# Performance work log

Measured on AMD Instinct MI355X. Metric: run time of the kernel, lower is better.

## Reference

```python
import jax, jax.numpy as jnp
import numpy as np

N_SVC = 100000
N_EP = 100000
E = 300000
D = 128
H = 128


def _sage(x_src, x_dst, edge_index, Wl, bl, Wr, n_dst):
    """PyG SAGEConv default: mean neighbor aggr, lin_l(aggr) + lin_r(x_dst)."""
    src, dst = edge_index[0], edge_index[1]
    msg = x_src[src]                                        # [E, D] gather
    sums = jax.ops.segment_sum(msg, dst, num_segments=n_dst)  # [n_dst, D]
    cnt = jax.ops.segment_sum(jnp.ones((msg.shape[0], 1), msg.dtype), dst,
                              num_segments=n_dst)             # [n_dst, 1]
    mean = sums / jnp.maximum(cnt, 1.0)
    return mean @ Wl.T + bl + x_dst @ Wr.T                  # [n_dst, H]


def setup_inputs() -> dict:
    key = jax.random.key(0)
    ks = jax.random.split(key, 16)
    scale = 1.0 / np.sqrt(D)
    inp = {
        "x_service": jax.random.normal(ks[0], (N_SVC, D), jnp.float32),
        "x_endpoint": jax.random.normal(ks[1], (N_EP, D), jnp.float32),
        "ei_calls": jax.random.randint(ks[2], (2, E), 0, N_SVC),   # svc -> svc
        "ei_has": jax.random.randint(ks[3], (2, E), 0, N_SVC),     # svc -> ep (dst < N_EP too)
        "ei_belongs": jax.random.randint(ks[4], (2, E), 0, N_EP),  # ep -> svc
        "Wl_calls": jax.random.normal(ks[5], (H, D), jnp.float32) * scale,
        "bl_calls": jnp.zeros((H,), jnp.float32),
        "Wr_calls": jax.random.normal(ks[6], (H, D), jnp.float32) * scale,
        "Wl_has": jax.random.normal(ks[7], (H, D), jnp.float32) * scale,
        "bl_has": jnp.zeros((H,), jnp.float32),
        "Wr_has": jax.random.normal(ks[8], (H, D), jnp.float32) * scale,
        "Wl_belongs": jax.random.normal(ks[9], (H, D), jnp.float32) * scale,
        "bl_belongs": jnp.zeros((H,), jnp.float32),
        "Wr_belongs": jax.random.normal(ks[10], (H, D), jnp.float32) * scale,
    }
    return inp


def reference(x_service, x_endpoint, ei_calls, ei_has, ei_belongs,
              Wl_calls, bl_calls, Wr_calls,
              Wl_has, bl_has, Wr_has,
              Wl_belongs, bl_belongs, Wr_belongs):
    # edge type (service, calls, service) -> service output
    out_calls = _sage(x_service, x_service, ei_calls, Wl_calls, bl_calls, Wr_calls, N_SVC)
    # edge type (endpoint, belongs, service) -> service output
    out_belongs = _sage(x_endpoint, x_service, ei_belongs, Wl_belongs, bl_belongs, Wr_belongs, N_SVC)
    # edge type (service, has, endpoint) -> endpoint output
    out_has = _sage(x_service, x_endpoint, ei_has, Wl_has, bl_has, Wr_has, N_EP)
    # HeteroConv aggr='sum': sum per destination node type
    out_service = out_calls + out_belongs
    out_endpoint = out_has
    return out_service, out_endpoint
```

## Files before the change

### kernel.cpp

```cpp
#include <hip/hip_runtime.h>

#define DF 128
#define CAP 24

typedef __bf16 bf16x8 __attribute__((ext_vector_type(8)));
typedef float f32x4 __attribute__((ext_vector_type(4)));
typedef unsigned short ushort8v __attribute__((ext_vector_type(8)));

__device__ __forceinline__ unsigned short f2bf(float f) {
    union { float f; unsigned int u; } v; v.f = f;
    unsigned int r = v.u + 0x7FFFu + ((v.u >> 16) & 1u);
    return (unsigned short)(r >> 16);
}
__device__ __forceinline__ float bf2f(unsigned short u) {
    union { unsigned int u; float f; } v; v.u = ((unsigned int)u) << 16;
    return v.f;
}

__global__ __launch_bounds__(256)
void prep_kernel(
                 const int* __restrict__ ei_calls, int E1,
                 const int* __restrict__ ei_belongs, int E2,
                 const int* __restrict__ ei_has, int E3,
                 int* __restrict__ cnt, int* __restrict__ slots,
                 const float* __restrict__ x_service,
                 const float* __restrict__ x_endpoint,
                 unsigned short* __restrict__ xb_svc,
                 unsigned short* __restrict__ xb_ep,
                 int n_svc, int n_ep,
                 const float* __restrict__ Wl_calls, const float* __restrict__ Wr_calls,
                 const float* __restrict__ Wl_belongs, const float* __restrict__ Wr_belongs,
                 const float* __restrict__ Wl_has, const float* __restrict__ Wr_has,
                 const float* __restrict__ bl_calls, const float* __restrict__ bl_belongs,
                 const float* __restrict__ bl_has,
                 unsigned short* __restrict__ Bp_svc, unsigned short* __restrict__ Bp_ep,
                 float* __restrict__ bias_svc, float* __restrict__ bias_ep,
                 int B_fill, int B_pack)
{
    int b = blockIdx.x;

    if (b < B_fill) {
        int e = b * 256 + threadIdx.x;
        int Etot = E1 + E2 + E3;
        if (e >= Etot) return;
        int s, d, base;
        if (e < E1)           { s = ei_calls[e]; d = ei_calls[E1 + e]; base = 0; }
        else if (e < E1 + E2) { int el = e - E1; s = ei_belongs[el]; d = ei_belongs[E2 + el]; base = n_svc; }
        else                  { int el = e - E1 - E2; s = ei_has[el]; d = ei_has[E3 + el]; base = 2 * n_svc; }
        int g = base + d;
        int pos = atomicAdd(cnt + g, 1);
        if (pos < CAP) slots[(size_t)g * CAP + pos] = s;
        return;
    }
    b -= B_fill;

    if (b < B_pack) {
        int t = b * 256 + threadIdx.x;
        const int SV = 12 * 8 * 64 * 8;
        const int EPN = 8 * 8 * 64 * 8;
        if (t < SV) {
            int j = t & 7, lane = (t >> 3) & 63, ct = (t >> 9) & 7, kt = t >> 12;
            int k = kt * 32 + (lane >> 4) * 8 + j;
            int n = ct * 16 + (lane & 15);
            float v;
            if (k < 128)       v = Wl_calls[n * DF + k];
            else if (k < 256)  v = Wl_belongs[n * DF + (k - 128)];
            else               v = Wr_calls[n * DF + (k - 256)] + Wr_belongs[n * DF + (k - 256)];
            Bp_svc[t] = f2bf(v);
        } else if (t < SV + EPN) {
            int t2 = t - SV;
            int j = t2 & 7, lane = (t2 >> 3) & 63, ct = (t2 >> 9) & 7, kt = t2 >> 12;
            int k = kt * 32 + (lane >> 4) * 8 + j;
            int n = ct * 16 + (lane & 15);
            float v = (k < 128) ? Wl_has[n * DF + k] : Wr_has[n * DF + (k - 128)];
            Bp_ep[t2] = f2bf(v);
        }
        if (t < 128) bias_svc[t] = bl_calls[t] + bl_belongs[t];
        else if (t < 256) bias_ep[t - 128] = bl_has[t - 128];
        return;
    }
    b -= B_pack;

    int tid = b * 256 + threadIdx.x;
    int node = tid >> 5;
    int c4 = (tid & 31) << 2;
    if (node < n_svc) {
        float4 v = *reinterpret_cast<const float4*>(x_service + (size_t)node * DF + c4);
        ushort4 o; o.x = f2bf(v.x); o.y = f2bf(v.y); o.z = f2bf(v.z); o.w = f2bf(v.w);
        *reinterpret_cast<ushort4*>(xb_svc + (size_t)node * DF + c4) = o;
    } else if (node < n_svc + n_ep) {
        int ne = node - n_svc;
        float4 v = *reinterpret_cast<const float4*>(x_endpoint + (size_t)ne * DF + c4);
        ushort4 o; o.x = f2bf(v.x); o.y = f2bf(v.y); o.z = f2bf(v.z); o.w = f2bf(v.w);
        *reinterpret_cast<ushort4*>(xb_ep + (size_t)ne * DF + c4) = o;
    }
}

template <int MODE>
__global__ __launch_bounds__(512, 4)
void fused_gemm(const unsigned short* __restrict__ xb_svc,
                const unsigned short* __restrict__ xb_ep,
                const int* __restrict__ cnt,
                const int* __restrict__ slots,
                const unsigned short* __restrict__ Bpack,
                const float* __restrict__ bias,
                float* __restrict__ out,
                int n_svc, int n_ep)
{
    constexpr int MK      = (MODE == 0) ? 256 : 128;
    constexpr int KSTEPS  = (MODE == 0) ? 12 : 8;
    constexpr int MKSTEPS = MK / 32;
    constexpr int ROWS    = 64;
    constexpr int NG      = (MODE == 0) ? 2 * ROWS : ROWS;
    constexpr int NI      = NG * 16 / 512;

    __shared__ unsigned short smean[ROWS * MK];

    const int M = (MODE == 0) ? n_svc : n_ep;
    const int row_base = blockIdx.x * ROWS;

    const int lane16 = threadIdx.x & 15;
    const int c8 = lane16 << 3;

    int degA[NI];
    int gA[NI];
    const unsigned short* srcA[NI];
    unsigned short* dstA[NI];

#pragma unroll
    for (int it = 0; it < NI; ++it) {
        int gl   = (it * 512 + threadIdx.x) >> 4;
        int node = gl & (ROWS - 1);
        int t    = gl / ROWS;
        int chunk = lane16 + t * 16;
        dstA[it] = smean + node * MK + ((chunk ^ (node & 7)) << 3);
        int gnode = row_base + node;
        int gn_c  = gnode < M ? gnode : M - 1;
        int g;
        if (MODE == 0) {
            g = (t == 0) ? gn_c : (n_svc + gn_c);
            srcA[it] = (t == 0) ? xb_svc : xb_ep;
        } else {
            g = 2 * n_svc + gn_c;
            srcA[it] = xb_svc;
        }
        gA[it] = g;
        int d = cnt[g];
        if (gnode >= M) d = 0;
        if (d > CAP) d = CAP;
        degA[it] = d;
    }

    int4 s4[NI];
#pragma unroll
    for (int it = 0; it < NI; ++it)
        s4[it] = *reinterpret_cast<const int4*>(slots + (size_t)gA[it] * CAP);

    int idxA[NI][4];
#pragma unroll
    for (int it = 0; it < NI; ++it) {
        int d = degA[it];
        idxA[it][0] = (0 < d) ? s4[it].x : 0;
        idxA[it][1] = (1 < d) ? s4[it].y : 0;
        idxA[it][2] = (2 < d) ? s4[it].z : 0;
        idxA[it][3] = (3 < d) ? s4[it].w : 0;
    }

    ushort8v vb0[4], vb1[4];
#pragma unroll
    for (int j = 0; j < 4; ++j)
        vb0[j] = *reinterpret_cast<const ushort8v*>(
            srcA[0] + (size_t)idxA[0][j] * DF + c8);

#pragma unroll
    for (int it = 0; it < NI; ++it) {
        if (it + 1 < NI) {
#pragma unroll
            for (int j = 0; j < 4; ++j) {
                const ushort8v* p = reinterpret_cast<const ushort8v*>(
                    srcA[it + 1] + (size_t)idxA[it + 1][j] * DF + c8);
                if ((it & 1) == 0) vb1[j] = *p; else vb0[j] = *p;
            }
        }
        float acc[8];
#pragma unroll
        for (int q = 0; q < 8; ++q) acc[q] = 0.f;
#pragma unroll
        for (int j = 0; j < 4; ++j) {
            if (j < degA[it]) {
                ushort8v v = ((it & 1) == 0) ? vb0[j] : vb1[j];
#pragma unroll
                for (int q = 0; q < 8; ++q) acc[q] += bf2f(v[q]);
            }
        }
        if (degA[it] <= 4) {
            float inv = 1.0f / (float)max(degA[it], 1);
            ushort8v o;
#pragma unroll
            for (int q = 0; q < 8; ++q) o[q] = f2bf(acc[q] * inv);
            *reinterpret_cast<ushort8v*>(dstA[it]) = o;
        }
    }

#pragma unroll
    for (int it = 0; it < NI; ++it) {
        int deg = degA[it];
        if (deg > 4) {
            const int* sp = slots + (size_t)gA[it] * CAP;
            const unsigned short* src = srcA[it];
            float acc[8];
#pragma unroll
            for (int q = 0; q < 8; ++q) acc[q] = 0.f;
            for (int i0 = 0; i0 < deg; i0 += 8) {
                int idx[8];
#pragma unroll
                for (int j = 0; j < 8; ++j) {
                    int ii = i0 + j;
                    if (ii > deg - 1) ii = deg - 1;
                    idx[j] = sp[ii];
                }
                ushort8v v[8];
#pragma unroll
                for (int j = 0; j < 8; ++j)
                    v[j] = *reinterpret_cast<const ushort8v*>(
                        src + (size_t)idx[j] * DF + c8);
                int nv = deg - i0;
#pragma unroll
                for (int j = 0; j < 8; ++j) {
                    if (j < nv) {
#pragma unroll
                        for (int q = 0; q < 8; ++q) acc[q] += bf2f(v[j][q]);
                    }
                }
            }
            float inv = 1.0f / (float)deg;
            ushort8v o;
#pragma unroll
            for (int q = 0; q < 8; ++q) o[q] = f2bf(acc[q] * inv);
            *reinterpret_cast<ushort8v*>(dstA[it]) = o;
        }
    }
    __syncthreads();

    const int lane = threadIdx.x & 63;
    const int wave = threadIdx.x >> 6;
    const int wr   = wave >> 2;
    const int wc   = wave & 3;
    const int quad = lane >> 4;
    const int lc   = lane & 15;
    const int m0l  = wr * 32 + lc;
    const int m1l  = m0l + 16;
    int m0 = row_base + m0l; if (m0 > M - 1) m0 = M - 1;
    int m1 = row_base + m1l; if (m1 > M - 1) m1 = M - 1;

    const unsigned short* xb_dst = (MODE == 0) ? xb_svc : xb_ep;
    const unsigned short* Xp0 = xb_dst + (size_t)m0 * DF + quad * 8;
    const unsigned short* Xp1 = xb_dst + (size_t)m1 * DF + quad * 8;
    const unsigned short* Bp  = Bpack + lane * 8 + (wc * 2) * 512;

    f32x4 acc0[2], acc1[2];
#pragma unroll
    for (int ct = 0; ct < 2; ++ct) {
        acc0[ct] = (f32x4){0.f, 0.f, 0.f, 0.f};
        acc1[ct] = (f32x4){0.f, 0.f, 0.f, 0.f};
    }

#pragma unroll
    for (int kt = 0; kt < KSTEPS; ++kt) {
        bf16x8 af0, af1;
        if (kt < MKSTEPS) {
            int c = kt * 4 + quad;
            af0 = *reinterpret_cast<const bf16x8*>(
                smean + m0l * MK + ((c ^ (m0l & 7)) << 3));
            af1 = *reinterpret_cast<const bf16x8*>(
                smean + m1l * MK + ((c ^ (m1l & 7)) << 3));
        } else {
            af0 = *reinterpret_cast<const bf16x8*>(Xp0 + (kt - MKSTEPS) * 32);
            af1 = *reinterpret_cast<const bf16x8*>(Xp1 + (kt - MKSTEPS) * 32);
        }
        const unsigned short* bptr = Bp + (size_t)kt * 8 * 512;
#pragma unroll
        for (int ct = 0; ct < 2; ++ct) {
            bf16x8 bf = *reinterpret_cast<const bf16x8*>(bptr + ct * 512);
            acc0[ct] = __builtin_amdgcn_mfma_f32_16x16x32_bf16(af0, bf, acc0[ct], 0, 0, 0);
            acc1[ct] = __builtin_amdgcn_mfma_f32_16x16x32_bf16(af1, bf, acc1[ct], 0, 0, 0);
        }
    }

    float bc[2];
#pragma unroll
    for (int ct = 0; ct < 2; ++ct) bc[ct] = bias[(wc * 2 + ct) * 16 + lc];

    const int row0 = row_base + wr * 32;
#pragma unroll
    for (int half = 0; half < 2; ++half) {
        int orow0 = row0 + half * 16 + quad * 4;
        f32x4* accp = half ? acc1 : acc0;
#pragma unroll
        for (int r = 0; r < 4; ++r) {
            int orow = orow0 + r;
            if (orow < M) {
                float* op = out + (size_t)orow * DF + wc * 32 + lc;
#pragma unroll
                for (int ct = 0; ct < 2; ++ct) op[ct * 16] = accp[ct][r] + bc[ct];
            }
        }
    }
}

extern "C" void kernel_launch(void* const* d_in, const int* in_sizes, int n_in,
                              void* d_out, int out_size, void* d_ws, size_t ws_size,
                              hipStream_t stream)
{
    const float* x_service  = (const float*)d_in[0];
    const float* x_endpoint = (const float*)d_in[1];
    const int*   ei_calls   = (const int*)d_in[2];
    const int*   ei_has     = (const int*)d_in[3];
    const int*   ei_belongs = (const int*)d_in[4];
    const float* Wl_calls   = (const float*)d_in[5];
    const float* bl_calls   = (const float*)d_in[6];
    const float* Wr_calls   = (const float*)d_in[7];
    const float* Wl_has     = (const float*)d_in[8];
    const float* bl_has     = (const float*)d_in[9];
    const float* Wr_has     = (const float*)d_in[10];
    const float* Wl_belongs = (const float*)d_in[11];
    const float* bl_belongs = (const float*)d_in[12];
    const float* Wr_belongs = (const float*)d_in[13];

    const int n_svc = in_sizes[0] / DF;
    const int n_ep  = in_sizes[1] / DF;
    const int E1 = in_sizes[2] / 2;
    const int E3 = in_sizes[3] / 2;
    const int E2 = in_sizes[4] / 2;
    const int Etot = E1 + E2 + E3;
    const int NT = 2 * n_svc + n_ep;

    int* wsi = (int*)d_ws;
    size_t oi = 0;
    int* cnt   = wsi + oi; oi += NT;
    int* slots = wsi + oi; oi += (size_t)NT * CAP;
    oi = (oi + 3) & ~(size_t)3;

    unsigned short* wsu = (unsigned short*)(wsi + oi);
    size_t ou = 0;
    unsigned short* xb_svc = wsu + ou; ou += (size_t)n_svc * DF;
    unsigned short* xb_ep  = wsu + ou; ou += (size_t)n_ep * DF;
    unsigned short* Bp_svc = wsu + ou; ou += 12 * 8 * 64 * 8;
    unsigned short* Bp_ep  = wsu + ou; ou += 8 * 8 * 64 * 8;
    ou = (ou + 7) & ~(size_t)7;
    float* bias_svc = (float*)(wsu + ou);
    float* bias_ep  = bias_svc + DF;

    hipMemsetAsync(cnt, 0, (size_t)NT * sizeof(int), stream);

    const int B_fill = (Etot + 255) / 256;
    const int B_pack = (12 * 8 * 64 * 8 + 8 * 8 * 64 * 8 + 255) / 256;
    const int B_conv = (int)(((size_t)(n_svc + n_ep) * 32 + 255) / 256);

    prep_kernel<<<B_fill + B_pack + B_conv, 256, 0, stream>>>(
        ei_calls, E1, ei_belongs, E2, ei_has, E3, cnt, slots,
        x_service, x_endpoint, xb_svc, xb_ep, n_svc, n_ep,
        Wl_calls, Wr_calls, Wl_belongs, Wr_belongs, Wl_has, Wr_has,
        bl_calls, bl_belongs, bl_has, Bp_svc, Bp_ep, bias_svc, bias_ep,
        B_fill, B_pack);

    float* out_svc = (float*)d_out;
    float* out_ep  = out_svc + (size_t)n_svc * DF;

    fused_gemm<0><<<(n_svc + 63) / 64, 512, 0, stream>>>(
        xb_svc, xb_ep, cnt, slots, Bp_svc, bias_svc, out_svc, n_svc, n_ep);
    fused_gemm<1><<<(n_ep + 63) / 64, 512, 0, stream>>>(
        xb_svc, xb_ep, cnt, slots, Bp_ep, bias_ep, out_ep, n_svc, n_ep);
}
```

Baseline: 365.7 us.

## Merge both GEMM launches into one interleaved grid and batch edge atomics

The two per-destination-type fused gather+GEMM kernels are combined into a single launch whose blocks alternate between service and endpoint tiles. This removes one launch and the tail gap between them, and mixes the heavier and lighter tiles across the GPU. The prep kernel now handles four edges per thread so several atomics are in flight at once. It also remaps block indices so the fill, pack and convert work is spread across the block range. The shared-memory array is now always sized for the larger service mode, which can reduce occupancy for endpoint blocks.

Result: slower. 681.5 us (+86.3%).

```diff
diff --git a/kernel.cpp b/kernel.cpp
--- a/kernel.cpp
+++ b/kernel.cpp
@@ -35,21 +35,35 @@
                  const float* __restrict__ bl_has,
                  unsigned short* __restrict__ Bp_svc, unsigned short* __restrict__ Bp_ep,
                  float* __restrict__ bias_svc, float* __restrict__ bias_ep,
-                 int B_fill, int B_pack)
+                 int B_fill, int B_pack, int B_tot)
 {
-    int b = blockIdx.x;
+    const int C = (B_tot + 31) >> 5;
+    int b = (blockIdx.x & 31) * C + (blockIdx.x >> 5);
+    if (b >= B_tot) return;
 
     if (b < B_fill) {
-        int e = b * 256 + threadIdx.x;
         int Etot = E1 + E2 + E3;
-        if (e >= Etot) return;
-        int s, d, base;
-        if (e < E1)           { s = ei_calls[e]; d = ei_calls[E1 + e]; base = 0; }
-        else if (e < E1 + E2) { int el = e - E1; s = ei_belongs[el]; d = ei_belongs[E2 + el]; base = n_svc; }
-        else                  { int el = e - E1 - E2; s = ei_has[el]; d = ei_has[E3 + el]; base = 2 * n_svc; }
-        int g = base + d;
-        int pos = atomicAdd(cnt + g, 1);
-        if (pos < CAP) slots[(size_t)g * CAP + pos] = s;
+        int e0 = (b * 256 + threadIdx.x) * 4;
+        int gl[4], sv[4];
+#pragma unroll
+        for (int j = 0; j < 4; ++j) {
+            int e = e0 + j;
+            if (e < Etot) {
+                int s, d, base;
+                if (e < E1)           { s = ei_calls[e]; d = ei_calls[E1 + e]; base = 0; }
+                else if (e < E1 + E2) { int el = e - E1; s = ei_belongs[el]; d = ei_belongs[E2 + el]; base = n_svc; }
+                else                  { int el = e - E1 - E2; s = ei_has[el]; d = ei_has[E3 + el]; base = 2 * n_svc; }
+                gl[j] = base + d; sv[j] = s;
+            } else gl[j] = -1;
+        }
+        int pos[4];
+#pragma unroll
+        for (int j = 0; j < 4; ++j)
+            if (gl[j] >= 0) pos[j] = atomicAdd(cnt + gl[j], 1);
+#pragma unroll
+        for (int j = 0; j < 4; ++j)
+            if (gl[j] >= 0 && pos[j] < CAP)
+                slots[(size_t)gl[j] * CAP + pos[j]] = sv[j];
         return;
     }
     b -= B_fill;
@@ -97,15 +111,16 @@
 }
 
 template <int MODE>
-__global__ __launch_bounds__(512, 4)
-void fused_gemm(const unsigned short* __restrict__ xb_svc,
-                const unsigned short* __restrict__ xb_ep,
-                const int* __restrict__ cnt,
-                const int* __restrict__ slots,
-                const unsigned short* __restrict__ Bpack,
-                const float* __restrict__ bias,
-                float* __restrict__ out,
-                int n_svc, int n_ep)
+__device__ __forceinline__ void fused_body(
+        int bid, unsigned short* __restrict__ smean,
+        const unsigned short* __restrict__ xb_svc,
+        const unsigned short* __restrict__ xb_ep,
+        const int* __restrict__ cnt,
+        const int* __restrict__ slots,
+        const unsigned short* __restrict__ Bpack,
+        const float* __restrict__ bias,
+        float* __restrict__ out,
+        int n_svc, int n_ep)
 {
     constexpr int MK      = (MODE == 0) ? 256 : 128;
     constexpr int KSTEPS  = (MODE == 0) ? 12 : 8;
@@ -114,10 +129,8 @@
     constexpr int NG      = (MODE == 0) ? 2 * ROWS : ROWS;
     constexpr int NI      = NG * 16 / 512;
 
-    __shared__ unsigned short smean[ROWS * MK];
-
     const int M = (MODE == 0) ? n_svc : n_ep;
-    const int row_base = blockIdx.x * ROWS;
+    const int row_base = bid * ROWS;
 
     const int lane16 = threadIdx.x & 15;
     const int c8 = lane16 << 3;
@@ -306,6 +319,39 @@
             }
         }
     }
+}
+
+__global__ __launch_bounds__(512, 4)
+void fused_gemm_all(const unsigned short* __restrict__ xb_svc,
+                    const unsigned short* __restrict__ xb_ep,
+                    const int* __restrict__ cnt,
+                    const int* __restrict__ slots,
+                    const unsigned short* __restrict__ Bp_svc,
+                    const unsigned short* __restrict__ Bp_ep,
+                    const float* __restrict__ bias_svc,
+                    const float* __restrict__ bias_ep,
+                    float* __restrict__ out_svc,
+                    float* __restrict__ out_ep,
+                    int n_svc, int n_ep, int G0, int G1)
+{
+    __shared__ unsigned short smean[64 * 256];
+
+    int b = blockIdx.x;
+    int Gm = (G0 < G1) ? G0 : G1;
+    int mode, idx;
+    if (b < 2 * Gm) { mode = b & 1; idx = b >> 1; }
+    else {
+        int r = b - 2 * Gm;
+        if (G0 > G1) { mode = 0; idx = Gm + r; }
+        else         { mode = 1; idx = Gm + r; }
+    }
+
+    if (mode == 0)
+        fused_body<0>(idx, smean, xb_svc, xb_ep, cnt, slots,
+                      Bp_svc, bias_svc, out_svc, n_svc, n_ep);
+    else
+        fused_body<1>(idx, smean, xb_svc, xb_ep, cnt, slots,
+                      Bp_ep, bias_ep, out_ep, n_svc, n_ep);
 }
 
 extern "C" void kernel_launch(void* const* d_in, const int* in_sizes, int n_in,
@@ -353,22 +399,26 @@
 
     hipMemsetAsync(cnt, 0, (size_t)NT * sizeof(int), stream);
 
-    const int B_fill = (Etot + 255) / 256;
+    const int B_fill = (Etot + 1023) / 1024;
     const int B_pack = (12 * 8 * 64 * 8 + 8 * 8 * 64 * 8 + 255) / 256;
     const int B_conv = (int)(((size_t)(n_svc + n_ep) * 32 + 255) / 256);
-
-    prep_kernel<<<B_fill + B_pack + B_conv, 256, 0, stream>>>(
+    const int B_tot  = B_fill + B_pack + B_conv;
+    const int C      = (B_tot + 31) >> 5;
+
+    prep_kernel<<<C * 32, 256, 0, stream>>>(
         ei_calls, E1, ei_belongs, E2, ei_has, E3, cnt, slots,
         x_service, x_endpoint, xb_svc, xb_ep, n_svc, n_ep,
         Wl_calls, Wr_calls, Wl_belongs, Wr_belongs, Wl_has, Wr_has,
         bl_calls, bl_belongs, bl_has, Bp_svc, Bp_ep, bias_svc, bias_ep,
-        B_fill, B_pack);
+        B_fill, B_pack, B_tot);
 
     float* out_svc = (float*)d_out;
     float* out_ep  = out_svc + (size_t)n_svc * DF;
 
-    fused_gemm<0><<<(n_svc + 63) / 64, 512, 0, stream>>>(
-        xb_svc, xb_ep, cnt, slots, Bp_svc, bias_svc, out_svc, n_svc, n_ep);
-    fused_gemm<1><<<(n_ep + 63) / 64, 512, 0, stream>>>(
-        xb_svc, xb_ep, cnt, slots, Bp_ep, bias_ep, out_ep, n_svc, n_ep);
-}
+    const int G0 = (n_svc + 63) / 64;
+    const int G1 = (n_ep + 63) / 64;
+
+    fused_gemm_all<<<G0 + G1, 512, 0, stream>>>(
+        xb_svc, xb_ep, cnt, slots, Bp_svc, Bp_ep,
+        bias_svc, bias_ep, out_svc, out_ep, n_svc, n_ep, G0, G1);
+}
```
